# Optimization experiments

Measured on AMD Instinct MI355X. Metric: run time of the kernel, lower is better.

Reference implementation:

```python
import jax, jax.numpy as jnp
import numpy as np

V, E, L = 32000, 512, 512
U = 2 * L  # GRU units = latent_dim * 2
B, T = 16, 128


def setup_inputs() -> dict:
    key = jax.random.key(0)
    ks = jax.random.split(key, 10)
    s = lambda k, shape, scale: jax.random.normal(k, shape, dtype=jnp.float32) * scale
    return {
        "latent_samples": jax.random.normal(ks[0], (B, L), dtype=jnp.float32),
        "true_outputs": jax.random.randint(ks[1], (B, T), 0, V, dtype=jnp.int32),
        "emb": s(ks[2], (V, E), 0.02),
        "W_dense": s(ks[3], (L, U), 0.02),
        "b_dense": jnp.zeros((U,), jnp.float32),
        "W_x": s(ks[4], (E, 3 * U), 0.02),   # GRU input kernel [z|r|h]
        "W_h": s(ks[5], (U, 3 * U), 0.02),   # GRU recurrent kernel [z|r|h]
        "b_x": jnp.zeros((3 * U,), jnp.float32),  # input bias (reset_after)
        "b_h": jnp.zeros((3 * U,), jnp.float32),  # recurrent bias (reset_after)
        "W_out": s(ks[6], (U, V), 0.02),
        "b_out": jnp.zeros((V,), jnp.float32),
    }


def _gru_scan(x_seq, mask_seq, h0, W_x, W_h, b_x, b_h):
    """x_seq: [B,T,E], mask_seq: [B,T] bool, h0: [B,U]. Keras GRU, reset_after=True."""
    # precompute input projections for all steps: [B,T,3U]
    xp = jnp.einsum('bte,eu->btu', x_seq, W_x) + b_x

    def step(h, inp):
        xp_t, m_t = inp  # [B,3U], [B]
        hp = h @ W_h + b_h  # [B,3U]
        xz, xr, xh = jnp.split(xp_t, 3, axis=-1)
        hz, hr, hh = jnp.split(hp, 3, axis=-1)
        z = jax.nn.sigmoid(xz + hz)
        r = jax.nn.sigmoid(xr + hr)
        hcand = jnp.tanh(xh + r * hh)
        h_new = z * h + (1.0 - z) * hcand
        h_out = jnp.where(m_t[:, None], h_new, h)  # masked steps carry state
        return h_out, h_out

    xs = (jnp.swapaxes(xp, 0, 1), jnp.swapaxes(mask_seq, 0, 1))
    _, hs = jax.lax.scan(step, h0, xs)
    return jnp.swapaxes(hs, 0, 1)  # [B,T,U]


def reference(latent_samples, true_outputs, emb, W_dense, b_dense,
              W_x, W_h, b_x, b_h, W_out, b_out):
    # teacher_forcing_decode with training=False (Dropout is identity)
    teacher = true_outputs[:, :-1]                  # [B,T-1]
    mask = teacher != 0                             # [B,T-1]
    x = emb[teacher]                                # [B,T-1,E]
    h0 = latent_samples @ W_dense + b_dense         # [B,U]
    gru_out = _gru_scan(x, mask, h0, W_x, W_h, b_x, b_h)  # [B,T-1,U]
    logits = jnp.einsum('btu,uv->btv', gru_out, W_out) + b_out  # [B,T-1,V]
    return logits
```

## Files before the change

kernel.cpp:

```cpp
#include <hip/hip_runtime.h>
#include <cstdint>
#include <cstddef>

#define DI static __device__ __forceinline__

typedef __bf16 bf16x8 __attribute__((ext_vector_type(8)));
typedef float  f32x4  __attribute__((ext_vector_type(4)));

DI ushort f2bf(float f) {
  uint32_t u = __float_as_uint(f);
  uint32_t r = (u + 0x7FFFu + ((u >> 16) & 1u)) >> 16;
  return (ushort)r;
}

__global__ __launch_bounds__(256) void k_dense_h0(const float* __restrict__ latent,
    const float* __restrict__ Wd, const float* __restrict__ bd, float* __restrict__ h0) {
  int b = blockIdx.x >> 2;
  int u = ((blockIdx.x & 3) << 8) + threadIdx.x;
  const float* lrow = latent + (b << 9);
  float acc = bd[u];
  #pragma unroll 8
  for (int k = 0; k < 512; ++k) acc = fmaf(lrow[k], Wd[((size_t)k << 10) + u], acc);
  h0[(b << 10) + u] = acc;
}

template<typename OutT>
__global__ __launch_bounds__(256) void k_transpose(const float* __restrict__ src,
    OutT* __restrict__ dst, int R, int C) {
  __shared__ float tile[32][33];
  int c0 = blockIdx.x << 5, r0 = blockIdx.y << 5;
  int tx = threadIdx.x, ty = threadIdx.y;
  #pragma unroll
  for (int i = 0; i < 32; i += 8)
    tile[ty + i][tx] = src[(size_t)(r0 + ty + i) * C + (c0 + tx)];
  __syncthreads();
  #pragma unroll
  for (int i = 0; i < 32; i += 8) {
    float v = tile[tx][ty + i];
    size_t o = (size_t)(c0 + ty + i) * R + (r0 + tx);
    if constexpr (sizeof(OutT) == 2) dst[o] = f2bf(v); else dst[o] = v;
  }
}

__global__ __launch_bounds__(256) void k_gather_x(const float* __restrict__ emb,
    const int* __restrict__ tok, ushort* __restrict__ xb) {
  int gid = (blockIdx.x << 8) + threadIdx.x;
  int m = gid >> 7, k4 = gid & 127;
  float4 v = make_float4(0.f, 0.f, 0.f, 0.f);
  if (m < 2032) {
    int b = m / 127, t = m - b * 127;
    int token = tok[(b << 7) + t];
    v = ((const float4*)(emb + ((size_t)token << 9)))[k4];
  }
  ushort4 o; o.x = f2bf(v.x); o.y = f2bf(v.y); o.z = f2bf(v.z); o.w = f2bf(v.w);
  ((ushort4*)xb)[gid] = o;
}

__global__ __launch_bounds__(256) void k_pad_hsb(ushort* __restrict__ hsb) {
  int row = 2032 + blockIdx.x;
  ushort4 z; z.x = 0; z.y = 0; z.z = 0; z.w = 0;
  ((ushort4*)(hsb + ((size_t)row << 10)))[threadIdx.x] = z;
}

__global__ __launch_bounds__(256) void k_gru_step(const float* __restrict__ h_cur,
    float* __restrict__ h_next, ushort* __restrict__ hsb, const float* __restrict__ xp,
    const float* __restrict__ WhT, const float* __restrict__ b_h,
    const int* __restrict__ tok, int t) {
  __shared__ __attribute__((aligned(16))) float hs[4 * 16 * 260];
  __shared__ float red[3][260];
  int tid = threadIdx.x;
  int lane = tid & 63, kq = tid >> 6;
  int b = tid & 15, ul = (tid >> 4) & 3;
  int u = (blockIdx.x << 2) + ul;
  int m = b * 127 + t;

  float xz = 0.f, xr = 0.f, xh = 0.f, bz = 0.f, br = 0.f, bhh = 0.f, hprev = 0.f;
  int tk = 1;
  if (kq == 0) {
    const float* xrow = xp + (size_t)m * 3072;
    xz = xrow[u]; xr = xrow[1024 + u]; xh = xrow[2048 + u];
    bz = b_h[u]; br = b_h[1024 + u]; bhh = b_h[2048 + u];
    hprev = h_cur[(b << 10) + u];
    tk = tok[(b << 7) + t];
  }

  float* hw = hs + kq * (16 * 260);
  const float4* hv = (const float4*)h_cur;
  #pragma unroll
  for (int i = 0; i < 16; ++i) {
    int idx = (i << 6) + lane;
    int bb = idx >> 6, kk = idx & 63;
    ((float4*)(hw + bb * 260))[kk] = hv[(bb << 8) + (kq << 6) + kk];
  }
  __syncthreads();

  const float4* h4 = (const float4*)(hw + b * 260);
  const float4* wz = (const float4*)(WhT + ((size_t)u << 10)) + (kq << 6);
  const float4* wr = (const float4*)(WhT + ((size_t)(1024 + u) << 10)) + (kq << 6);
  const float4* wh = (const float4*)(WhT + ((size_t)(2048 + u) << 10)) + (kq << 6);
  float az = 0.f, ar = 0.f, ah = 0.f;
  #pragma unroll 8
  for (int k = 0; k < 64; ++k) {
    float4 h = h4[k];
    float4 a = wz[k], e = wr[k], c = wh[k];
    az = fmaf(h.x, a.x, fmaf(h.y, a.y, fmaf(h.z, a.z, fmaf(h.w, a.w, az))));
    ar = fmaf(h.x, e.x, fmaf(h.y, e.y, fmaf(h.z, e.z, fmaf(h.w, e.w, ar))));
    ah = fmaf(h.x, c.x, fmaf(h.y, c.y, fmaf(h.z, c.z, fmaf(h.w, c.w, ah))));
  }
  red[0][tid] = az; red[1][tid] = ar; red[2][tid] = ah;
  __syncthreads();

  if (tid < 64) {
    az = red[0][tid] + red[0][tid + 64] + red[0][tid + 128] + red[0][tid + 192];
    ar = red[1][tid] + red[1][tid + 64] + red[1][tid + 128] + red[1][tid + 192];
    ah = red[2][tid] + red[2][tid + 64] + red[2][tid + 128] + red[2][tid + 192];
    float z = 1.f / (1.f + __expf(-(xz + az + bz)));
    float r = 1.f / (1.f + __expf(-(xr + ar + br)));
    float hc = tanhf(xh + r * (ah + bhh));
    float hn = z * hprev + (1.f - z) * hc;
    if (tk == 0) hn = hprev;
    h_next[(b << 10) + u] = hn;
    hsb[((size_t)m << 10) + u] = f2bf(hn);
  }
}

__global__ __launch_bounds__(256) void k_gemm_bf16(const ushort* __restrict__ A,
    const ushort* __restrict__ BT, const float* __restrict__ bias, float* __restrict__ C,
    int M, int N, int K, int Mreal, int MT) {
  __shared__ __attribute__((aligned(16))) ushort ldsA[128 * 64];
  __shared__ __attribute__((aligned(16))) ushort ldsB[128 * 64];
  int nwg = gridDim.x;
  int q = nwg >> 3;
  int swz = (blockIdx.x & 7) * q + (blockIdx.x >> 3);
  int m0 = (swz % MT) << 7;
  int n0 = (swz / MT) << 7;
  int tid = threadIdx.x;
  int lane = tid & 63, wave = tid >> 6;
  int wm = (wave >> 1) << 6, wn = (wave & 1) << 6;
  f32x4 acc[4][4] = {};
  const char* Ab = (const char*)A;
  const char* Bb = (const char*)BT;
  size_t stride = (size_t)K * 2;

  for (int k0 = 0; k0 < K; k0 += 64) {
    #pragma unroll
    for (int it = 0; it < 4; ++it) {
      int c = (it << 8) + tid;
      int row = c >> 3;
      int cb = ((c & 7) << 4) ^ ((row & 7) << 4);
      const char* ga = Ab + (size_t)(m0 + row) * stride + (size_t)(k0 << 1) + cb;
      const char* gb = Bb + (size_t)(n0 + row) * stride + (size_t)(k0 << 1) + cb;
      __builtin_amdgcn_global_load_lds((const __attribute__((address_space(1))) void*)ga,
          (__attribute__((address_space(3))) void*)(ldsA + (((it << 2) + wave) << 9)), 16, 0, 0);
      __builtin_amdgcn_global_load_lds((const __attribute__((address_space(1))) void*)gb,
          (__attribute__((address_space(3))) void*)(ldsB + (((it << 2) + wave) << 9)), 16, 0, 0);
    }
    __syncthreads();
    #pragma unroll
    for (int kk = 0; kk < 2; ++kk) {
      bf16x8 av[4], bv[4];
      int kb = (kk << 6) + ((lane >> 4) << 4);
      #pragma unroll
      for (int f = 0; f < 4; ++f) {
        int ra = wm + (f << 4) + (lane & 15);
        av[f] = *(const bf16x8*)((const char*)ldsA + ra * 128 + (kb ^ ((ra & 7) << 4)));
        int rb = wn + (f << 4) + (lane & 15);
        bv[f] = *(const bf16x8*)((const char*)ldsB + rb * 128 + (kb ^ ((rb & 7) << 4)));
      }
      #pragma unroll
      for (int fm = 0; fm < 4; ++fm)
        #pragma unroll
        for (int fn = 0; fn < 4; ++fn)
          acc[fm][fn] = __builtin_amdgcn_mfma_f32_16x16x32_bf16(av[fm], bv[fn], acc[fm][fn], 0, 0, 0);
    }
    __syncthreads();
  }

  #pragma unroll
  for (int fn = 0; fn < 4; ++fn) {
    int n = n0 + wn + (fn << 4) + (lane & 15);
    float bvs = bias ? bias[n] : 0.f;
    #pragma unroll
    for (int fm = 0; fm < 4; ++fm) {
      int mbase = m0 + wm + (fm << 4) + ((lane >> 4) << 2);
      #pragma unroll
      for (int r = 0; r < 4; ++r) {
        int m = mbase + r;
        if (m < Mreal) C[(size_t)m * N + n] = acc[fm][fn][r] + bvs;
      }
    }
  }
}

extern "C" void kernel_launch(void* const* d_in, const int* in_sizes, int n_in,
                              void* d_out, int out_size, void* d_ws, size_t ws_size,
                              hipStream_t stream) {
  (void)in_sizes; (void)n_in; (void)out_size; (void)ws_size;
  const float* latent = (const float*)d_in[0];
  const int*   tok    = (const int*)d_in[1];
  const float* emb    = (const float*)d_in[2];
  const float* Wd     = (const float*)d_in[3];
  const float* bd     = (const float*)d_in[4];
  const float* Wx     = (const float*)d_in[5];
  const float* Wh     = (const float*)d_in[6];
  const float* bx     = (const float*)d_in[7];
  const float* bh     = (const float*)d_in[8];
  const float* Wout   = (const float*)d_in[9];
  const float* bout   = (const float*)d_in[10];
  float* out = (float*)d_out;

  char* w = (char*)d_ws;
  float*  h0v = (float*)(w + 0);
  float*  h1v = (float*)(w + 65536);
  float*  WhT = (float*)(w + 131072);
  float*  xp  = (float*)(w + 12713984);
  ushort* xb  = (ushort*)(w + 37683200);
  ushort* WxT = (ushort*)(w + 39780352);
  ushort* hsb = (ushort*)(w + 42926080);
  ushort* WoT = (ushort*)(w + 47120384);

  k_transpose<float ><<<dim3(96, 32),   dim3(32, 8), 0, stream>>>(Wh,   WhT, 1024, 3072);
  k_transpose<ushort><<<dim3(96, 16),   dim3(32, 8), 0, stream>>>(Wx,   WxT,  512, 3072);
  k_transpose<ushort><<<dim3(1000, 32), dim3(32, 8), 0, stream>>>(Wout, WoT, 1024, 32000);

  k_dense_h0<<<64, 256, 0, stream>>>(latent, Wd, bd, h0v);
  k_gather_x<<<1024, 256, 0, stream>>>(emb, tok, xb);
  k_pad_hsb<<<16, 256, 0, stream>>>(hsb);

  k_gemm_bf16<<<384, 256, 0, stream>>>(xb, WxT, bx, xp, 2048, 3072, 512, 2032, 16);

  float* hc = h0v; float* hn = h1v;
  for (int t = 0; t < 127; ++t) {
    k_gru_step<<<256, 256, 0, stream>>>(hc, hn, hsb, xp, WhT, bh, tok, t);
    float* tmp = hc; hc = hn; hn = tmp;
  }

  k_gemm_bf16<<<4000, 256, 0, stream>>>(hsb, WoT, bout, out, 2048, 32000, 1024, 2032, 16);
}
```

Measured before the change: 1.852 ms.

## Fuse GRU recurrence into one persistent kernel with grid barrier and LDS-resident weights

```diff
diff --git a/kernel.cpp b/kernel.cpp
--- a/kernel.cpp
+++ b/kernel.cpp
@@ -62,65 +62,104 @@
   ((ushort4*)(hsb + ((size_t)row << 10)))[threadIdx.x] = z;
 }
 
-__global__ __launch_bounds__(256) void k_gru_step(const float* __restrict__ h_cur,
-    float* __restrict__ h_next, ushort* __restrict__ hsb, const float* __restrict__ xp,
-    const float* __restrict__ WhT, const float* __restrict__ b_h,
-    const int* __restrict__ tok, int t) {
-  __shared__ __attribute__((aligned(16))) float hs[4 * 16 * 260];
-  __shared__ float red[3][260];
+__global__ __launch_bounds__(256) void k_scan(
+    const float* __restrict__ WhT, const float* __restrict__ xp,
+    const float* __restrict__ b_h, const int* __restrict__ tok,
+    float* __restrict__ hb0, float* __restrict__ hb1,
+    ushort* __restrict__ hsb, unsigned* __restrict__ bar) {
+  extern __shared__ float lds[];
+  float* Wl  = lds;
+  float* hl  = lds + 12 * 1028;
+  float* red = lds + 12 * 1028 + 16 * 1028;
+
   int tid = threadIdx.x;
-  int lane = tid & 63, kq = tid >> 6;
-  int b = tid & 15, ul = (tid >> 4) & 3;
-  int u = (blockIdx.x << 2) + ul;
-  int m = b * 127 + t;
-
-  float xz = 0.f, xr = 0.f, xh = 0.f, bz = 0.f, br = 0.f, bhh = 0.f, hprev = 0.f;
-  int tk = 1;
-  if (kq == 0) {
-    const float* xrow = xp + (size_t)m * 3072;
-    xz = xrow[u]; xr = xrow[1024 + u]; xh = xrow[2048 + u];
-    bz = b_h[u]; br = b_h[1024 + u]; bhh = b_h[2048 + u];
-    hprev = h_cur[(b << 10) + u];
-    tk = tok[(b << 7) + t];
-  }
-
-  float* hw = hs + kq * (16 * 260);
-  const float4* hv = (const float4*)h_cur;
-  #pragma unroll
-  for (int i = 0; i < 16; ++i) {
-    int idx = (i << 6) + lane;
-    int bb = idx >> 6, kk = idx & 63;
-    ((float4*)(hw + bb * 260))[kk] = hv[(bb << 8) + (kq << 6) + kk];
-  }
+  int bl = blockIdx.x;
+  int u0 = bl << 2;
+  int b = tid & 15, ul = (tid >> 4) & 3, kq = tid >> 6;
+  int u = u0 + ul;
+
+  for (int f = tid; f < 3072; f += 256) {
+    int row12 = f >> 8, col4 = f & 255;
+    int g = row12 >> 2, uu = row12 & 3;
+    float4 v = ((const float4*)(WhT + ((size_t)((g << 10) + u0 + uu) << 10)))[col4];
+    ((float4*)(Wl + (size_t)row12 * 1028))[col4] = v;
+  }
+  float bz = 0.f, brr = 0.f, bhh = 0.f;
+  if (kq == 0) { bz = b_h[u]; brr = b_h[1024 + u]; bhh = b_h[2048 + u]; }
   __syncthreads();
 
-  const float4* h4 = (const float4*)(hw + b * 260);
-  const float4* wz = (const float4*)(WhT + ((size_t)u << 10)) + (kq << 6);
-  const float4* wr = (const float4*)(WhT + ((size_t)(1024 + u) << 10)) + (kq << 6);
-  const float4* wh = (const float4*)(WhT + ((size_t)(2048 + u) << 10)) + (kq << 6);
-  float az = 0.f, ar = 0.f, ah = 0.f;
-  #pragma unroll 8
-  for (int k = 0; k < 64; ++k) {
-    float4 h = h4[k];
-    float4 a = wz[k], e = wr[k], c = wh[k];
-    az = fmaf(h.x, a.x, fmaf(h.y, a.y, fmaf(h.z, a.z, fmaf(h.w, a.w, az))));
-    ar = fmaf(h.x, e.x, fmaf(h.y, e.y, fmaf(h.z, e.z, fmaf(h.w, e.w, ar))));
-    ah = fmaf(h.x, c.x, fmaf(h.y, c.y, fmaf(h.z, c.z, fmaf(h.w, c.w, ah))));
-  }
-  red[0][tid] = az; red[1][tid] = ar; red[2][tid] = ah;
-  __syncthreads();
-
-  if (tid < 64) {
-    az = red[0][tid] + red[0][tid + 64] + red[0][tid + 128] + red[0][tid + 192];
-    ar = red[1][tid] + red[1][tid + 64] + red[1][tid + 128] + red[1][tid + 192];
-    ah = red[2][tid] + red[2][tid + 64] + red[2][tid + 128] + red[2][tid + 192];
-    float z = 1.f / (1.f + __expf(-(xz + az + bz)));
-    float r = 1.f / (1.f + __expf(-(xr + ar + br)));
-    float hc = tanhf(xh + r * (ah + bhh));
-    float hn = z * hprev + (1.f - z) * hc;
-    if (tk == 0) hn = hprev;
-    h_next[(b << 10) + u] = hn;
-    hsb[((size_t)m << 10) + u] = f2bf(hn);
+  const float4* w0 = (const float4*)(Wl + (size_t)(0 + ul) * 1028) + (kq << 6);
+  const float4* w1 = (const float4*)(Wl + (size_t)(4 + ul) * 1028) + (kq << 6);
+  const float4* w2 = (const float4*)(Wl + (size_t)(8 + ul) * 1028) + (kq << 6);
+  const float4* h4base = (const float4*)(hl + (size_t)b * 1028) + (kq << 6);
+
+  for (int t = 0; t < 127; ++t) {
+    const float* hc = (t & 1) ? hb1 : hb0;
+    float*       hn = (t & 1) ? hb0 : hb1;
+    int m = b * 127 + t;
+
+    float xz = 0.f, xr = 0.f, xh = 0.f, hprev = 0.f; int tk = 1;
+    if (kq == 0) {
+      const float* xrow = xp + (size_t)m * 3072;
+      xz = xrow[u]; xr = xrow[1024 + u]; xh = xrow[2048 + u];
+      hprev = hc[(b << 10) + u];
+      tk = tok[(b << 7) + t];
+    }
+
+    #pragma unroll
+    for (int i = 0; i < 16; ++i) {
+      int f = (i << 8) + tid;
+      ((float4*)(hl + (size_t)i * 1028))[tid] = ((const float4*)hc)[f];
+    }
+    __syncthreads();
+
+    float az0 = 0.f, az1 = 0.f, ar0 = 0.f, ar1 = 0.f, ah0 = 0.f, ah1 = 0.f;
+    #pragma unroll 8
+    for (int k = 0; k < 64; k += 2) {
+      float4 h = h4base[k], a = w0[k], e = w1[k], c = w2[k];
+      az0 = fmaf(h.x, a.x, fmaf(h.y, a.y, fmaf(h.z, a.z, fmaf(h.w, a.w, az0))));
+      ar0 = fmaf(h.x, e.x, fmaf(h.y, e.y, fmaf(h.z, e.z, fmaf(h.w, e.w, ar0))));
+      ah0 = fmaf(h.x, c.x, fmaf(h.y, c.y, fmaf(h.z, c.z, fmaf(h.w, c.w, ah0))));
+      float4 h2 = h4base[k + 1], a2 = w0[k + 1], e2 = w1[k + 1], c2 = w2[k + 1];
+      az1 = fmaf(h2.x, a2.x, fmaf(h2.y, a2.y, fmaf(h2.z, a2.z, fmaf(h2.w, a2.w, az1))));
+      ar1 = fmaf(h2.x, e2.x, fmaf(h2.y, e2.y, fmaf(h2.z, e2.z, fmaf(h2.w, e2.w, ar1))));
+      ah1 = fmaf(h2.x, c2.x, fmaf(h2.y, c2.y, fmaf(h2.z, c2.z, fmaf(h2.w, c2.w, ah1))));
+    }
+    red[tid] = az0 + az1; red[256 + tid] = ar0 + ar1; red[512 + tid] = ah0 + ah1;
+    __syncthreads();
+
+    if (tid < 64) {
+      float az = red[tid] + red[tid + 64] + red[tid + 128] + red[tid + 192];
+      float ar = red[256 + tid] + red[256 + tid + 64] + red[256 + tid + 128] + red[256 + tid + 192];
+      float ah = red[512 + tid] + red[512 + tid + 64] + red[512 + tid + 128] + red[512 + tid + 192];
+      float z = 1.f / (1.f + __expf(-(xz + az + bz)));
+      float r = 1.f / (1.f + __expf(-(xr + ar + brr)));
+      float hcand = tanhf(xh + r * (ah + bhh));
+      float v = z * hprev + (1.f - z) * hcand;
+      if (tk == 0) v = hprev;
+      hn[(b << 10) + u] = v;
+      hsb[((size_t)m << 10) + u] = f2bf(v);
+    }
+    __syncthreads();
+
+    if (t < 126) {
+      if (tid == 0) {
+        int g = bl >> 4;
+        unsigned old = __hip_atomic_fetch_add(&bar[g * 32], 1u,
+                         __ATOMIC_ACQ_REL, __HIP_MEMORY_SCOPE_AGENT);
+        if ((old & 15u) == 15u)
+          __hip_atomic_fetch_add(&bar[16 * 32], 1u,
+                         __ATOMIC_ACQ_REL, __HIP_MEMORY_SCOPE_AGENT);
+        unsigned target = (unsigned)(t + 1) << 4;
+        int spins = 0;
+        while (__hip_atomic_load(&bar[16 * 32], __ATOMIC_ACQUIRE,
+                                 __HIP_MEMORY_SCOPE_AGENT) < target) {
+          __builtin_amdgcn_s_sleep(2);
+          if (++spins > 60000) break;
+        }
+      }
+      __syncthreads();
+    }
   }
 }
 
@@ -210,30 +249,32 @@
   float* out = (float*)d_out;
 
   char* w = (char*)d_ws;
-  float*  h0v = (float*)(w + 0);
-  float*  h1v = (float*)(w + 65536);
-  float*  WhT = (float*)(w + 131072);
-  float*  xp  = (float*)(w + 12713984);
-  ushort* xb  = (ushort*)(w + 37683200);
-  ushort* WxT = (ushort*)(w + 39780352);
-  ushort* hsb = (ushort*)(w + 42926080);
-  ushort* WoT = (ushort*)(w + 47120384);
+  float*    hb0 = (float*)(w + 0);
+  float*    hb1 = (float*)(w + 65536);
+  unsigned* bar = (unsigned*)(w + 131072);
+  float*    WhT = (float*)(w + 135168);
+  float*    xp  = (float*)(w + 12718080);
+  ushort*   xb  = (ushort*)(w + 37883904);
+  ushort*   WxT = (ushort*)(w + 39981056);
+  ushort*   hsb = (ushort*)(w + 43126784);
+  ushort*   WoT = (ushort*)(w + 47321088);
+
+  (void)hipFuncSetAttribute((const void*)k_scan,
+      hipFuncAttributeMaxDynamicSharedMemorySize, 118272);
+
+  (void)hipMemsetAsync(bar, 0, 4096, stream);
 
   k_transpose<float ><<<dim3(96, 32),   dim3(32, 8), 0, stream>>>(Wh,   WhT, 1024, 3072);
   k_transpose<ushort><<<dim3(96, 16),   dim3(32, 8), 0, stream>>>(Wx,   WxT,  512, 3072);
   k_transpose<ushort><<<dim3(1000, 32), dim3(32, 8), 0, stream>>>(Wout, WoT, 1024, 32000);
 
-  k_dense_h0<<<64, 256, 0, stream>>>(latent, Wd, bd, h0v);
+  k_dense_h0<<<64, 256, 0, stream>>>(latent, Wd, bd, hb0);
   k_gather_x<<<1024, 256, 0, stream>>>(emb, tok, xb);
   k_pad_hsb<<<16, 256, 0, stream>>>(hsb);
 
   k_gemm_bf16<<<384, 256, 0, stream>>>(xb, WxT, bx, xp, 2048, 3072, 512, 2032, 16);
 
-  float* hc = h0v; float* hn = h1v;
-  for (int t = 0; t < 127; ++t) {
-    k_gru_step<<<256, 256, 0, stream>>>(hc, hn, hsb, xp, WhT, bh, tok, t);
-    float* tmp = hc; hc = hn; hn = tmp;
-  }
+  k_scan<<<256, 256, 118272, stream>>>(WhT, xp, bh, tok, hb0, hb1, hsb, bar);
 
   k_gemm_bf16<<<4000, 256, 0, stream>>>(hsb, WoT, bout, out, 2048, 32000, 1024, 2032, 16);
 }
```

Result: slower. 3.793 ms (+104.9%).
